# Optimization experiments

Hardware: AMD Instinct MI355X
Metric: run time of the kernel (lower is better)

## Reference

```python
import jax, jax.numpy as jnp
import numpy as np

H = 12          # num_attention_heads
DH = 64         # attention_head_size (768/12)
LDH = 16        # layout head size (DH / channel_shrink_ratio=4)


def _split_heads(x, h, d):
    # [B,S,h*d] -> [B,h,S,d]
    B, S, _ = x.shape
    return x.reshape(B, S, h, d).transpose(0, 2, 1, 3)


def setup_inputs() -> dict:
    key = jax.random.key(0)
    ks = jax.random.split(key, 16)
    B, S, D, LD = 4, 2048, 768, 192
    std = 0.02
    inp = {
        "hidden_states": jax.random.normal(ks[0], (B, S, D), jnp.float32),
        "layout_hidden_states": jax.random.normal(ks[1], (B, S, LD), jnp.float32),
        "attention_mask": jnp.zeros((B, 1, 1, S), jnp.float32),
        # text-stream QKV (weights stored [in, out] so y = x @ W + b)
        "Wq": jax.random.normal(ks[2], (D, D), jnp.float32) * std,
        "bq": jnp.zeros((D,), jnp.float32),
        "Wk": jax.random.normal(ks[3], (D, D), jnp.float32) * std,
        "bk": jnp.zeros((D,), jnp.float32),
        "Wv": jax.random.normal(ks[4], (D, D), jnp.float32) * std,
        "bv": jnp.zeros((D,), jnp.float32),
        # layout-stream QKV
        "LWq": jax.random.normal(ks[5], (LD, LD), jnp.float32) * std,
        "Lbq": jnp.zeros((LD,), jnp.float32),
        "LWk": jax.random.normal(ks[6], (LD, LD), jnp.float32) * std,
        "Lbk": jnp.zeros((LD,), jnp.float32),
        "LWv": jax.random.normal(ks[7], (LD, LD), jnp.float32) * std,
        "Lbv": jnp.zeros((LD,), jnp.float32),
    }
    return inp


def reference(hidden_states, layout_hidden_states, attention_mask,
              Wq, bq, Wk, bk, Wv, bv, LWq, Lbq, LWk, Lbk, LWv, Lbv):
    B, S, D = hidden_states.shape
    LD = layout_hidden_states.shape[-1]

    q = _split_heads(hidden_states @ Wq + bq, H, DH)   # [B,H,S,DH]
    k = _split_heads(hidden_states @ Wk + bk, H, DH)
    v = _split_heads(hidden_states @ Wv + bv, H, DH)
    lq = _split_heads(layout_hidden_states @ LWq + Lbq, H, LDH)  # [B,H,S,LDH]
    lk = _split_heads(layout_hidden_states @ LWk + Lbk, H, LDH)
    lv = _split_heads(layout_hidden_states @ LWv + Lbv, H, LDH)

    # scaled per-stream scores
    scores_t = jnp.einsum('bhqd,bhkd->bhqk', q, k) / np.sqrt(DH).astype(np.float32)
    scores_l = jnp.einsum('bhqd,bhkd->bhqk', lq, lk) / np.sqrt(LDH).astype(np.float32)

    # bidirectional cross-addition (BiACM); layout branch detaches the text scores
    scores_text = scores_t + scores_l + attention_mask
    scores_layout = jax.lax.stop_gradient(scores_t) + scores_l + attention_mask

    probs_t = jax.nn.softmax(scores_text, axis=-1)
    probs_l = jax.nn.softmax(scores_layout, axis=-1)

    ctx = jnp.einsum('bhqk,bhkd->bhqd', probs_t, v)
    ctx = ctx.transpose(0, 2, 1, 3).reshape(B, S, H * DH)       # [B,S,768]
    lctx = jnp.einsum('bhqk,bhkd->bhqd', probs_l, lv)
    lctx = lctx.transpose(0, 2, 1, 3).reshape(B, S, H * LDH)    # [B,S,192]
    return (ctx, lctx)
```

## Files before the change

### kernel.cpp

```cpp
#include <hip/hip_runtime.h>
#include <hip/hip_bf16.h>
#include <cstdint>
#include <math.h>

typedef __attribute__((ext_vector_type(8))) short bf16x8;
typedef __attribute__((ext_vector_type(4))) float f32x4;

#define MFMA16(a, b, c) __builtin_amdgcn_mfma_f32_16x16x32_bf16((a), (b), (c), 0, 0, 0)

static __device__ __forceinline__ unsigned short f2b(float x) {
  __hip_bfloat16 h = __float2bfloat16(x);
  return __builtin_bit_cast(unsigned short, h);
}

#define INVLN2 1.4426950408889634f

__global__ __launch_bounds__(256) void cvt_f32_bf16(const float* __restrict__ s,
                                                    __hip_bfloat16* __restrict__ d, int n) {
  int stride = gridDim.x * 256 * 4;
  for (int i = (blockIdx.x * 256 + threadIdx.x) * 4; i < n; i += stride) {
    float4 v = *(const float4*)(s + i);
    ushort4 o;
    o.x = f2b(v.x); o.y = f2b(v.y); o.z = f2b(v.z); o.w = f2b(v.w);
    *(ushort4*)&d[i] = o;
  }
}

__global__ __launch_bounds__(256) void transpose_cvt(const float* __restrict__ s0,
                                                     const float* __restrict__ s1,
                                                     const float* __restrict__ s2,
                                                     __hip_bfloat16* __restrict__ dst,
                                                     int K, int N, int Npad) {
  __shared__ float tile[32][33];
  int p = blockIdx.z;
  const float* src = (p == 0) ? s0 : (p == 1) ? s1 : s2;
  int n0 = blockIdx.x * 32, k0 = blockIdx.y * 32;
  int tx = threadIdx.x & 31, ty = threadIdx.x >> 5;
  for (int i = ty; i < 32; i += 8) {
    int k = k0 + i, n = n0 + tx;
    tile[i][tx] = (k < K && n < N) ? src[(size_t)k * N + n] : 0.f;
  }
  __syncthreads();
  for (int i = ty; i < 32; i += 8) {
    int n = n0 + i, k = k0 + tx;
    if (n < Npad && k < K)
      dst[(size_t)p * Npad * K + (size_t)n * K + k] = __float2bfloat16(tile[tx][i]);
  }
}

template <int K, int N, int NPAD, int HD, int COFF>
__global__ __launch_bounds__(256, 2) void proj_gemm(
    const __hip_bfloat16* __restrict__ X, const __hip_bfloat16* __restrict__ Wt,
    const float* __restrict__ bq, const float* __restrict__ bk, const float* __restrict__ bv,
    __hip_bfloat16* __restrict__ qc, __hip_bfloat16* __restrict__ kc,
    __hip_bfloat16* __restrict__ vt, float qscale) {
  __shared__ __hip_bfloat16 lA[128 * 32];
  __shared__ __hip_bfloat16 lB[128 * 32];
  const int tid = threadIdx.x, w = tid >> 6, l = tid & 63;
  const int lr = l & 15, lg = l >> 4;
  const int p = blockIdx.z;
  const int m0 = blockIdx.x * 128, n0 = blockIdx.y * 128;
  const __hip_bfloat16* Wp = Wt + (size_t)p * NPAD * K;
  const float* bias = (p == 0) ? bq : (p == 1) ? bk : bv;
  const float scale = (p == 0) ? qscale : 1.0f;

  f32x4 acc[4][4] = {};

  const int srow = (w * 2) * 16 + (l >> 2);
  const int scol = (l & 3) * 8;
  const __hip_bfloat16* gA = X + (size_t)(m0 + srow) * K + scol;
  const __hip_bfloat16* gB = Wp + (size_t)(n0 + srow) * K + scol;
  __hip_bfloat16* dA = lA + (w * 2) * 512;
  __hip_bfloat16* dB = lB + (w * 2) * 512;
  const int wr = w >> 1, wc = w & 1;

  for (int kk = 0; kk < K; kk += 32) {
    __builtin_amdgcn_global_load_lds((const __attribute__((address_space(1))) void*)(gA + kk),
                                     (__attribute__((address_space(3))) void*)dA, 16, 0, 0);
    __builtin_amdgcn_global_load_lds((const __attribute__((address_space(1))) void*)(gA + (size_t)16 * K + kk),
                                     (__attribute__((address_space(3))) void*)(dA + 512), 16, 0, 0);
    __builtin_amdgcn_global_load_lds((const __attribute__((address_space(1))) void*)(gB + kk),
                                     (__attribute__((address_space(3))) void*)dB, 16, 0, 0);
    __builtin_amdgcn_global_load_lds((const __attribute__((address_space(1))) void*)(gB + (size_t)16 * K + kk),
                                     (__attribute__((address_space(3))) void*)(dB + 512), 16, 0, 0);
    __syncthreads();
    bf16x8 af[4], bfr[4];
#pragma unroll
    for (int i = 0; i < 4; i++) af[i] = *(const bf16x8*)(lA + (wr * 64 + i * 16 + lr) * 32 + lg * 8);
#pragma unroll
    for (int j = 0; j < 4; j++) bfr[j] = *(const bf16x8*)(lB + (wc * 64 + j * 16 + lr) * 32 + lg * 8);
#pragma unroll
    for (int i = 0; i < 4; i++)
#pragma unroll
      for (int j = 0; j < 4; j++) acc[i][j] = MFMA16(bfr[j], af[i], acc[i][j]);
    __syncthreads();
  }

#pragma unroll
  for (int j = 0; j < 4; j++) {
    int nb = n0 + wc * 64 + j * 16 + lg * 4;
    if (NPAD > N && nb >= N) continue;
    float4 bv4 = *(const float4*)(bias + nb);
    int hh = nb / HD, d0 = nb % HD;
#pragma unroll
    for (int i = 0; i < 4; i++) {
      int m = m0 + wr * 64 + i * 16 + lr;
      int bb = m >> 11, s = m & 2047;
      if (p == 2) {
        size_t based = ((size_t)(bb * 12 + hh) * 80 + COFF + d0) * 2048 + s;
        vt[based]          = __float2bfloat16(acc[i][j][0] + bv4.x);
        vt[based + 2048]   = __float2bfloat16(acc[i][j][1] + bv4.y);
        vt[based + 4096]   = __float2bfloat16(acc[i][j][2] + bv4.z);
        vt[based + 6144]   = __float2bfloat16(acc[i][j][3] + bv4.w);
      } else {
        size_t base = ((size_t)(bb * 12 + hh) * 2048 + s) * 80 + COFF + d0;
        ushort4 st;
        st.x = f2b((acc[i][j][0] + bv4.x) * scale);
        st.y = f2b((acc[i][j][1] + bv4.y) * scale);
        st.z = f2b((acc[i][j][2] + bv4.z) * scale);
        st.w = f2b((acc[i][j][3] + bv4.w) * scale);
        *(ushort4*)((p == 0 ? qc : kc) + base) = st;
      }
    }
  }
}

__global__ __launch_bounds__(256, 3) void attn_kernel(
    const __hip_bfloat16* __restrict__ qc, const __hip_bfloat16* __restrict__ kc,
    const __hip_bfloat16* __restrict__ vt, const float* __restrict__ mask,
    float* __restrict__ out, float* __restrict__ out2) {
  constexpr int KP = 88;
  constexpr int VP = 72;
  constexpr int SP = 72;
  __shared__ __hip_bfloat16 lK[64 * KP];
  __shared__ __hip_bfloat16 lV[96 * VP];
  __shared__ __hip_bfloat16 lP[4 * 32 * SP];
  const int tid = threadIdx.x, w = tid >> 6, l = tid & 63;
  const int lr = l & 15, lg = l >> 4;
  const int bh = blockIdx.y, b_ = bh / 12, h = bh - b_ * 12;
  const int q0 = blockIdx.x * 128;

  const __hip_bfloat16* gsrc[5];
  int gstep[5];
  __hip_bfloat16* ldst[5];
#pragma unroll
  for (int s = 0; s < 5; ++s) {
    int idx = tid + s * 256;
    if (idx < 640) {
      int r = idx / 10, c = idx - r * 10;
      gsrc[s] = kc + ((size_t)bh * 2048 + r) * 80 + c * 8;
      gstep[s] = 64 * 80;
      ldst[s] = lK + r * KP + c * 8;
    } else {
      int vi = idx - 640;
      int r = vi >> 3, c = vi & 7;
      gsrc[s] = vt + ((size_t)bh * 80 + r) * 2048 + c * 8;
      gstep[s] = 64;
      ldst[s] = lV + r * VP + c * 8;
    }
  }

  const bf16x8 zz = {0, 0, 0, 0, 0, 0, 0, 0};
  bf16x8 aq[2][3];
#pragma unroll
  for (int g = 0; g < 2; ++g) {
    const __hip_bfloat16* qrow = qc + ((size_t)bh * 2048 + q0 + w * 32 + g * 16 + lr) * 80;
    aq[g][0] = *(const bf16x8*)(qrow + lg * 8);
    aq[g][1] = *(const bf16x8*)(qrow + 32 + lg * 8);
    bf16x8 t = *(const bf16x8*)(qrow + 64 + (lg & 1) * 8);
    aq[g][2] = (lg < 2) ? t : zz;
  }

  if (tid < 128) {
    int r = 80 + (tid >> 3), c = tid & 7;
    short v = (r == 80) ? (short)0x3F80 : (short)0;
    bf16x8 x = {v, v, v, v, v, v, v, v};
    *(bf16x8*)(lV + r * VP + c * 8) = x;
  }
  {
    bf16x8 r0[5];
#pragma unroll
    for (int s = 0; s < 5; ++s) r0[s] = *(const bf16x8*)(gsrc[s]);
#pragma unroll
    for (int s = 0; s < 5; ++s) *(bf16x8*)(ldst[s]) = r0[s];
  }
  __syncthreads();

  float mrun[2] = {-INFINITY, -INFINITY};
  f32x4 o[2][6] = {};
  const float* maskb = mask + b_ * 2048;
  __hip_bfloat16* SPw = lP + w * 32 * SP;

  for (int kt = 0; kt < 32; ++kt) {
    int ktn = (kt + 1 < 32) ? kt + 1 : 31;
    bf16x8 pre[5];
#pragma unroll
    for (int s = 0; s < 5; ++s)
      pre[s] = *(const bf16x8*)(gsrc[s] + (size_t)ktn * gstep[s]);

    const int kv0 = kt * 64;

    f32x4 sf[2][4] = {};
#pragma unroll
    for (int f = 0; f < 4; ++f) {
      const __hip_bfloat16* kr = lK + (f * 16 + lr) * KP;
      bf16x8 b0 = *(const bf16x8*)(kr + lg * 8);
      bf16x8 b1 = *(const bf16x8*)(kr + 32 + lg * 8);
      bf16x8 bt = *(const bf16x8*)(kr + 64 + (lg & 1) * 8);
      bf16x8 b2 = (lg < 2) ? bt : zz;
#pragma unroll
      for (int g = 0; g < 2; ++g) {
        sf[g][f] = MFMA16(b0, aq[g][0], sf[g][f]);
        sf[g][f] = MFMA16(b1, aq[g][1], sf[g][f]);
        sf[g][f] = MFMA16(b2, aq[g][2], sf[g][f]);
      }
    }
#pragma unroll
    for (int f = 0; f < 4; ++f) {
      float4 mv = *(const float4*)(maskb + kv0 + f * 16 + lg * 4);
#pragma unroll
      for (int g = 0; g < 2; ++g) {
        sf[g][f][0] += mv.x * INVLN2;
        sf[g][f][1] += mv.y * INVLN2;
        sf[g][f][2] += mv.z * INVLN2;
        sf[g][f][3] += mv.w * INVLN2;
      }
    }
    float tm[2];
#pragma unroll
    for (int g = 0; g < 2; ++g) {
      float a01 = fmaxf(fmaxf(sf[g][0][0], sf[g][0][1]), fmaxf(sf[g][0][2], sf[g][0][3]));
      float a23 = fmaxf(fmaxf(sf[g][1][0], sf[g][1][1]), fmaxf(sf[g][1][2], sf[g][1][3]));
      float a45 = fmaxf(fmaxf(sf[g][2][0], sf[g][2][1]), fmaxf(sf[g][2][2], sf[g][2][3]));
      float a67 = fmaxf(fmaxf(sf[g][3][0], sf[g][3][1]), fmaxf(sf[g][3][2], sf[g][3][3]));
      float m = fmaxf(fmaxf(a01, a23), fmaxf(a45, a67));
      m = fmaxf(m, __shfl_xor(m, 16));
      m = fmaxf(m, __shfl_xor(m, 32));
      tm[g] = m;
    }
    if (__any((tm[0] > mrun[0] + 8.f) || (tm[1] > mrun[1] + 8.f))) {
      float nm0 = fmaxf(mrun[0], tm[0]), nm1 = fmaxf(mrun[1], tm[1]);
      float a0 = exp2f(mrun[0] - nm0), a1 = exp2f(mrun[1] - nm1);
      mrun[0] = nm0; mrun[1] = nm1;
      float aO0[4], aO1[4];
#pragma unroll
      for (int j = 0; j < 4; ++j) {
        aO0[j] = __shfl(a0, lg * 4 + j);
        aO1[j] = __shfl(a1, lg * 4 + j);
      }
#pragma unroll
      for (int c = 0; c < 6; ++c)
#pragma unroll
        for (int j = 0; j < 4; ++j) {
          o[0][c][j] *= aO0[j];
          o[1][c][j] *= aO1[j];
        }
    }
#pragma unroll
    for (int g = 0; g < 2; ++g)
#pragma unroll
      for (int f = 0; f < 4; ++f) {
        ushort4 pk;
        pk.x = f2b(exp2f(sf[g][f][0] - mrun[g]));
        pk.y = f2b(exp2f(sf[g][f][1] - mrun[g]));
        pk.z = f2b(exp2f(sf[g][f][2] - mrun[g]));
        pk.w = f2b(exp2f(sf[g][f][3] - mrun[g]));
        *(ushort4*)(SPw + (g * 16 + lr) * SP + f * 16 + lg * 4) = pk;
      }

#pragma unroll
    for (int t2 = 0; t2 < 2; ++t2) {
      bf16x8 pa0 = *(const bf16x8*)(SPw + lr * SP + t2 * 32 + lg * 8);
      bf16x8 pa1 = *(const bf16x8*)(SPw + (16 + lr) * SP + t2 * 32 + lg * 8);
#pragma unroll
      for (int c = 0; c < 6; ++c) {
        bf16x8 bv_ = *(const bf16x8*)(lV + (c * 16 + lr) * VP + t2 * 32 + lg * 8);
        o[0][c] = MFMA16(pa0, bv_, o[0][c]);
        o[1][c] = MFMA16(pa1, bv_, o[1][c]);
      }
    }
    __syncthreads();
#pragma unroll
    for (int s = 0; s < 5; ++s) *(bf16x8*)(ldst[s]) = pre[s];
    __syncthreads();
  }

#pragma unroll
  for (int g = 0; g < 2; ++g) {
#pragma unroll
    for (int j = 0; j < 4; ++j) {
      float den = __shfl(o[g][5][j], (l & 48));
      float inv = 1.0f / den;
      int qg = q0 + w * 32 + g * 16 + lg * 4 + j;
      float* ob = out + ((size_t)b_ * 2048 + qg) * 768 + h * 64;
#pragma unroll
      for (int c = 0; c < 4; ++c) ob[c * 16 + lr] = o[g][c][j] * inv;
      out2[((size_t)b_ * 2048 + qg) * 192 + h * 16 + lr] = o[g][4][j] * inv;
    }
  }
}

extern "C" void kernel_launch(void* const* d_in, const int* in_sizes, int n_in,
                              void* d_out, int out_size, void* d_ws, size_t ws_size,
                              hipStream_t stream) {
  const float* hidden = (const float*)d_in[0];
  const float* lhidden = (const float*)d_in[1];
  const float* mask = (const float*)d_in[2];
  const float* Wq = (const float*)d_in[3];
  const float* bq = (const float*)d_in[4];
  const float* Wk = (const float*)d_in[5];
  const float* bk = (const float*)d_in[6];
  const float* Wv = (const float*)d_in[7];
  const float* bv = (const float*)d_in[8];
  const float* LWq = (const float*)d_in[9];
  const float* Lbq = (const float*)d_in[10];
  const float* LWk = (const float*)d_in[11];
  const float* Lbk = (const float*)d_in[12];
  const float* LWv = (const float*)d_in[13];
  const float* Lbv = (const float*)d_in[14];

  char* ws = (char*)d_ws;
  __hip_bfloat16* Xb  = (__hip_bfloat16*)(ws + 0);
  __hip_bfloat16* LXb = (__hip_bfloat16*)(ws + 12582912);
  __hip_bfloat16* Wt  = (__hip_bfloat16*)(ws + 15728640);
  __hip_bfloat16* LWt = (__hip_bfloat16*)(ws + 19267584);
  __hip_bfloat16* qcb = (__hip_bfloat16*)(ws + 19562496);
  __hip_bfloat16* kcb = (__hip_bfloat16*)(ws + 35291136);
  __hip_bfloat16* vtb = (__hip_bfloat16*)(ws + 51019776);

  float* out = (float*)d_out;
  float* out2 = out + (size_t)4 * 2048 * 768;

  cvt_f32_bf16<<<2048, 256, 0, stream>>>(hidden, Xb, 6291456);
  cvt_f32_bf16<<<1024, 256, 0, stream>>>(lhidden, LXb, 1572864);
  transpose_cvt<<<dim3(24, 24, 3), 256, 0, stream>>>(Wq, Wk, Wv, Wt, 768, 768, 768);
  transpose_cvt<<<dim3(8, 6, 3), 256, 0, stream>>>(LWq, LWk, LWv, LWt, 192, 192, 256);

  proj_gemm<768, 768, 768, 64, 0><<<dim3(64, 6, 3), 256, 0, stream>>>(
      Xb, Wt, bq, bk, bv, qcb, kcb, vtb, 0.125f * INVLN2);
  proj_gemm<192, 192, 256, 16, 64><<<dim3(64, 2, 3), 256, 0, stream>>>(
      LXb, LWt, Lbq, Lbk, Lbv, qcb, kcb, vtb, 0.25f * INVLN2);

  attn_kernel<<<dim3(16, 48), 256, 0, stream>>>(qcb, kcb, vtb, mask, out, out2);
}
```

Baseline: 319.7 us.

## Rewrite attention loop with 32x32 MFMA, double-buffered LDS and register-resident P

Rewrites the attention kernel to use 32x32x16 bf16 MFMAs instead of 16x16x32, so each wave handles 32 queries with one running max per lane. K tiles are double-buffered in LDS via direct global-to-LDS loads, and V tiles are prefetched into a second buffer. This removes one barrier per iteration and the LDS round-trip for the probability matrix, since the score accumulator layout feeds the PV MFMA directly from registers. LDS use and register pressure change, which may affect occupancy at 3 blocks per CU, and the V staging writes use narrower 8-byte stores.

```diff
diff --git a/kernel.cpp b/kernel.cpp
--- a/kernel.cpp
+++ b/kernel.cpp
@@ -4,13 +4,21 @@
 #include <math.h>
 
 typedef __attribute__((ext_vector_type(8))) short bf16x8;
+typedef __attribute__((ext_vector_type(4))) short bf16x4;
 typedef __attribute__((ext_vector_type(4))) float f32x4;
+typedef __attribute__((ext_vector_type(16))) float f32x16;
 
 #define MFMA16(a, b, c) __builtin_amdgcn_mfma_f32_16x16x32_bf16((a), (b), (c), 0, 0, 0)
+#define MFMA32(a, b, c) __builtin_amdgcn_mfma_f32_32x32x16_bf16((a), (b), (c), 0, 0, 0)
 
 static __device__ __forceinline__ unsigned short f2b(float x) {
   __hip_bfloat16 h = __float2bfloat16(x);
   return __builtin_bit_cast(unsigned short, h);
+}
+
+static __device__ __forceinline__ void gload16(const void* g, void* l) {
+  __builtin_amdgcn_global_load_lds((const __attribute__((address_space(1))) void*)g,
+                                   (__attribute__((address_space(3))) void*)l, 16, 0, 0);
 }
 
 #define INVLN2 1.4426950408889634f
@@ -75,14 +83,10 @@
   const int wr = w >> 1, wc = w & 1;
 
   for (int kk = 0; kk < K; kk += 32) {
-    __builtin_amdgcn_global_load_lds((const __attribute__((address_space(1))) void*)(gA + kk),
-                                     (__attribute__((address_space(3))) void*)dA, 16, 0, 0);
-    __builtin_amdgcn_global_load_lds((const __attribute__((address_space(1))) void*)(gA + (size_t)16 * K + kk),
-                                     (__attribute__((address_space(3))) void*)(dA + 512), 16, 0, 0);
-    __builtin_amdgcn_global_load_lds((const __attribute__((address_space(1))) void*)(gB + kk),
-                                     (__attribute__((address_space(3))) void*)dB, 16, 0, 0);
-    __builtin_amdgcn_global_load_lds((const __attribute__((address_space(1))) void*)(gB + (size_t)16 * K + kk),
-                                     (__attribute__((address_space(3))) void*)(dB + 512), 16, 0, 0);
+    gload16(gA + kk, dA);
+    gload16(gA + (size_t)16 * K + kk, dA + 512);
+    gload16(gB + kk, dB);
+    gload16(gB + (size_t)16 * K + kk, dB + 512);
     __syncthreads();
     bf16x8 af[4], bfr[4];
 #pragma unroll
@@ -129,174 +133,157 @@
     const __hip_bfloat16* __restrict__ qc, const __hip_bfloat16* __restrict__ kc,
     const __hip_bfloat16* __restrict__ vt, const float* __restrict__ mask,
     float* __restrict__ out, float* __restrict__ out2) {
-  constexpr int KP = 88;
-  constexpr int VP = 72;
-  constexpr int SP = 72;
-  __shared__ __hip_bfloat16 lK[64 * KP];
-  __shared__ __hip_bfloat16 lV[96 * VP];
-  __shared__ __hip_bfloat16 lP[4 * 32 * SP];
+  __shared__ __hip_bfloat16 lK[2][10 * 512];
+  __shared__ __hip_bfloat16 lV[2][8 * 776];
   const int tid = threadIdx.x, w = tid >> 6, l = tid & 63;
-  const int lr = l & 15, lg = l >> 4;
+  const int hi = l >> 5, ln = l & 31;
   const int bh = blockIdx.y, b_ = bh / 12, h = bh - b_ * 12;
   const int q0 = blockIdx.x * 128;
 
-  const __hip_bfloat16* gsrc[5];
-  int gstep[5];
-  __hip_bfloat16* ldst[5];
-#pragma unroll
-  for (int s = 0; s < 5; ++s) {
-    int idx = tid + s * 256;
-    if (idx < 640) {
-      int r = idx / 10, c = idx - r * 10;
-      gsrc[s] = kc + ((size_t)bh * 2048 + r) * 80 + c * 8;
-      gstep[s] = 64 * 80;
-      ldst[s] = lK + r * KP + c * 8;
-    } else {
-      int vi = idx - 640;
-      int r = vi >> 3, c = vi & 7;
-      gsrc[s] = vt + ((size_t)bh * 80 + r) * 2048 + c * 8;
-      gstep[s] = 64;
-      ldst[s] = lV + r * VP + c * 8;
-    }
-  }
-
-  const bf16x8 zz = {0, 0, 0, 0, 0, 0, 0, 0};
-  bf16x8 aq[2][3];
-#pragma unroll
-  for (int g = 0; g < 2; ++g) {
-    const __hip_bfloat16* qrow = qc + ((size_t)bh * 2048 + q0 + w * 32 + g * 16 + lr) * 80;
-    aq[g][0] = *(const bf16x8*)(qrow + lg * 8);
-    aq[g][1] = *(const bf16x8*)(qrow + 32 + lg * 8);
-    bf16x8 t = *(const bf16x8*)(qrow + 64 + (lg & 1) * 8);
-    aq[g][2] = (lg < 2) ? t : zz;
-  }
-
-  if (tid < 128) {
-    int r = 80 + (tid >> 3), c = tid & 7;
-    short v = (r == 80) ? (short)0x3F80 : (short)0;
+  const __hip_bfloat16* kbase = kc + ((size_t)bh * 2048 + l) * 80;
+  const __hip_bfloat16* vbase = vt + (size_t)bh * 80 * 2048;
+  const float* maskb = mask + b_ * 2048;
+
+  const int vd0 = tid >> 3, va0 = tid & 7;
+  const int vd1 = (tid + 256) >> 3, va1 = tid & 7;
+  const int vd2 = (tid + 512) >> 3, va2 = tid & 7;
+
+  bf16x8 aq[5];
+  {
+    const __hip_bfloat16* qp = qc + ((size_t)bh * 2048 + q0 + w * 32 + ln) * 80 + hi * 8;
+#pragma unroll
+    for (int t = 0; t < 5; ++t) aq[t] = *(const bf16x8*)(qp + t * 16);
+  }
+
+  {
+    int buf = tid >> 7, g = (tid >> 4) & 7, row = 80 + (tid & 15);
+    short v = (row == 80) ? (short)0x3F80 : (short)0;
     bf16x8 x = {v, v, v, v, v, v, v, v};
-    *(bf16x8*)(lV + r * VP + c * 8) = x;
+    *(bf16x8*)(&lV[buf][g * 776 + row * 8]) = x;
   }
   {
-    bf16x8 r0[5];
-#pragma unroll
-    for (int s = 0; s < 5; ++s) r0[s] = *(const bf16x8*)(gsrc[s]);
-#pragma unroll
-    for (int s = 0; s < 5; ++s) *(bf16x8*)(ldst[s]) = r0[s];
+    const __hip_bfloat16* kg = kbase;
+    gload16(kg + w * 8, &lK[0][w * 512]);
+    gload16(kg + (4 + w) * 8, &lK[0][(4 + w) * 512]);
+    if (w < 2) gload16(kg + (8 + w) * 8, &lK[0][(8 + w) * 512]);
+    bf16x8 v0 = *(const bf16x8*)(vbase + (size_t)vd0 * 2048 + va0 * 8);
+    bf16x8 v1 = *(const bf16x8*)(vbase + (size_t)vd1 * 2048 + va1 * 8);
+    *(bf16x4*)(&lV[0][(va0 & 6) * 776 + vd0 * 8 + (va0 & 1) * 4]) = bf16x4{v0[0], v0[1], v0[2], v0[3]};
+    *(bf16x4*)(&lV[0][((va0 & 6) | 1) * 776 + vd0 * 8 + (va0 & 1) * 4]) = bf16x4{v0[4], v0[5], v0[6], v0[7]};
+    *(bf16x4*)(&lV[0][(va1 & 6) * 776 + vd1 * 8 + (va1 & 1) * 4]) = bf16x4{v1[0], v1[1], v1[2], v1[3]};
+    *(bf16x4*)(&lV[0][((va1 & 6) | 1) * 776 + vd1 * 8 + (va1 & 1) * 4]) = bf16x4{v1[4], v1[5], v1[6], v1[7]};
+    if (tid < 128) {
+      bf16x8 v2 = *(const bf16x8*)(vbase + (size_t)vd2 * 2048 + va2 * 8);
+      *(bf16x4*)(&lV[0][(va2 & 6) * 776 + vd2 * 8 + (va2 & 1) * 4]) = bf16x4{v2[0], v2[1], v2[2], v2[3]};
+      *(bf16x4*)(&lV[0][((va2 & 6) | 1) * 776 + vd2 * 8 + (va2 & 1) * 4]) = bf16x4{v2[4], v2[5], v2[6], v2[7]};
+    }
   }
   __syncthreads();
 
-  float mrun[2] = {-INFINITY, -INFINITY};
-  f32x4 o[2][6] = {};
-  const float* maskb = mask + b_ * 2048;
-  __hip_bfloat16* SPw = lP + w * 32 * SP;
+  float mrun = -INFINITY;
+  f32x16 o0 = {}, o1 = {}, o2 = {};
 
   for (int kt = 0; kt < 32; ++kt) {
-    int ktn = (kt + 1 < 32) ? kt + 1 : 31;
-    bf16x8 pre[5];
-#pragma unroll
-    for (int s = 0; s < 5; ++s)
-      pre[s] = *(const bf16x8*)(gsrc[s] + (size_t)ktn * gstep[s]);
-
+    const int cur = kt & 1, nxt = cur ^ 1;
+    const int kvn = (kt + 1 < 32) ? (kt + 1) * 64 : kt * 64;
     const int kv0 = kt * 64;
 
-    f32x4 sf[2][4] = {};
-#pragma unroll
-    for (int f = 0; f < 4; ++f) {
-      const __hip_bfloat16* kr = lK + (f * 16 + lr) * KP;
-      bf16x8 b0 = *(const bf16x8*)(kr + lg * 8);
-      bf16x8 b1 = *(const bf16x8*)(kr + 32 + lg * 8);
-      bf16x8 bt = *(const bf16x8*)(kr + 64 + (lg & 1) * 8);
-      bf16x8 b2 = (lg < 2) ? bt : zz;
-#pragma unroll
-      for (int g = 0; g < 2; ++g) {
-        sf[g][f] = MFMA16(b0, aq[g][0], sf[g][f]);
-        sf[g][f] = MFMA16(b1, aq[g][1], sf[g][f]);
-        sf[g][f] = MFMA16(b2, aq[g][2], sf[g][f]);
-      }
-    }
-#pragma unroll
-    for (int f = 0; f < 4; ++f) {
-      float4 mv = *(const float4*)(maskb + kv0 + f * 16 + lg * 4);
-#pragma unroll
-      for (int g = 0; g < 2; ++g) {
-        sf[g][f][0] += mv.x * INVLN2;
-        sf[g][f][1] += mv.y * INVLN2;
-        sf[g][f][2] += mv.z * INVLN2;
-        sf[g][f][3] += mv.w * INVLN2;
-      }
-    }
-    float tm[2];
-#pragma unroll
-    for (int g = 0; g < 2; ++g) {
-      float a01 = fmaxf(fmaxf(sf[g][0][0], sf[g][0][1]), fmaxf(sf[g][0][2], sf[g][0][3]));
-      float a23 = fmaxf(fmaxf(sf[g][1][0], sf[g][1][1]), fmaxf(sf[g][1][2], sf[g][1][3]));
-      float a45 = fmaxf(fmaxf(sf[g][2][0], sf[g][2][1]), fmaxf(sf[g][2][2], sf[g][2][3]));
-      float a67 = fmaxf(fmaxf(sf[g][3][0], sf[g][3][1]), fmaxf(sf[g][3][2], sf[g][3][3]));
-      float m = fmaxf(fmaxf(a01, a23), fmaxf(a45, a67));
-      m = fmaxf(m, __shfl_xor(m, 16));
-      m = fmaxf(m, __shfl_xor(m, 32));
-      tm[g] = m;
-    }
-    if (__any((tm[0] > mrun[0] + 8.f) || (tm[1] > mrun[1] + 8.f))) {
-      float nm0 = fmaxf(mrun[0], tm[0]), nm1 = fmaxf(mrun[1], tm[1]);
-      float a0 = exp2f(mrun[0] - nm0), a1 = exp2f(mrun[1] - nm1);
-      mrun[0] = nm0; mrun[1] = nm1;
-      float aO0[4], aO1[4];
-#pragma unroll
-      for (int j = 0; j < 4; ++j) {
-        aO0[j] = __shfl(a0, lg * 4 + j);
-        aO1[j] = __shfl(a1, lg * 4 + j);
-      }
-#pragma unroll
-      for (int c = 0; c < 6; ++c)
-#pragma unroll
-        for (int j = 0; j < 4; ++j) {
-          o[0][c][j] *= aO0[j];
-          o[1][c][j] *= aO1[j];
-        }
-    }
-#pragma unroll
-    for (int g = 0; g < 2; ++g)
-#pragma unroll
-      for (int f = 0; f < 4; ++f) {
-        ushort4 pk;
-        pk.x = f2b(exp2f(sf[g][f][0] - mrun[g]));
-        pk.y = f2b(exp2f(sf[g][f][1] - mrun[g]));
-        pk.z = f2b(exp2f(sf[g][f][2] - mrun[g]));
-        pk.w = f2b(exp2f(sf[g][f][3] - mrun[g]));
-        *(ushort4*)(SPw + (g * 16 + lr) * SP + f * 16 + lg * 4) = pk;
-      }
-
-#pragma unroll
-    for (int t2 = 0; t2 < 2; ++t2) {
-      bf16x8 pa0 = *(const bf16x8*)(SPw + lr * SP + t2 * 32 + lg * 8);
-      bf16x8 pa1 = *(const bf16x8*)(SPw + (16 + lr) * SP + t2 * 32 + lg * 8);
-#pragma unroll
-      for (int c = 0; c < 6; ++c) {
-        bf16x8 bv_ = *(const bf16x8*)(lV + (c * 16 + lr) * VP + t2 * 32 + lg * 8);
-        o[0][c] = MFMA16(pa0, bv_, o[0][c]);
-        o[1][c] = MFMA16(pa1, bv_, o[1][c]);
-      }
+    {
+      const __hip_bfloat16* kg = kbase + (size_t)kvn * 80;
+      gload16(kg + w * 8, &lK[nxt][w * 512]);
+      gload16(kg + (4 + w) * 8, &lK[nxt][(4 + w) * 512]);
+      if (w < 2) gload16(kg + (8 + w) * 8, &lK[nxt][(8 + w) * 512]);
+    }
+    bf16x8 v0 = *(const bf16x8*)(vbase + (size_t)vd0 * 2048 + kvn + va0 * 8);
+    bf16x8 v1 = *(const bf16x8*)(vbase + (size_t)vd1 * 2048 + kvn + va1 * 8);
+    bf16x8 v2;
+    if (tid < 128) v2 = *(const bf16x8*)(vbase + (size_t)vd2 * 2048 + kvn + va2 * 8);
+
+    const __hip_bfloat16* lKc = &lK[cur][0];
+    f32x16 sf0 = {}, sf1 = {};
+#pragma unroll
+    for (int t = 0; t < 5; ++t) {
+      bf16x8 ak0 = *(const bf16x8*)(lKc + (t * 2 + hi) * 512 + ln * 8);
+      bf16x8 ak1 = *(const bf16x8*)(lKc + (t * 2 + hi) * 512 + (32 + ln) * 8);
+      sf0 = MFMA32(ak0, aq[t], sf0);
+      sf1 = MFMA32(ak1, aq[t], sf1);
+    }
+
+    float s_[2][16];
+#pragma unroll
+    for (int q = 0; q < 4; ++q) {
+      float4 m0 = *(const float4*)(maskb + kv0 + 4 * hi + q * 8);
+      float4 m1 = *(const float4*)(maskb + kv0 + 32 + 4 * hi + q * 8);
+#pragma unroll
+      for (int c = 0; c < 4; ++c) {
+        s_[0][q * 4 + c] = sf0[q * 4 + c] + ((const float*)&m0)[c] * INVLN2;
+        s_[1][q * 4 + c] = sf1[q * 4 + c] + ((const float*)&m1)[c] * INVLN2;
+      }
+    }
+
+    float tm = s_[0][0];
+#pragma unroll
+    for (int r = 1; r < 16; ++r) tm = fmaxf(tm, s_[0][r]);
+#pragma unroll
+    for (int r = 0; r < 16; ++r) tm = fmaxf(tm, s_[1][r]);
+    tm = fmaxf(tm, __shfl_xor(tm, 32));
+    if (__any(tm > mrun + 8.f)) {
+      float nm = fmaxf(mrun, tm);
+      float alpha = exp2f(mrun - nm);
+      mrun = nm;
+#pragma unroll
+      for (int r = 0; r < 16; ++r) {
+        float a = __shfl(alpha, (r & 3) + 8 * (r >> 2) + 4 * hi);
+        o0[r] *= a; o1[r] *= a; o2[r] *= a;
+      }
+    }
+
+    bf16x8 pa[2][2];
+#pragma unroll
+    for (int kb = 0; kb < 2; ++kb)
+#pragma unroll
+      for (int ks = 0; ks < 2; ++ks) {
+        bf16x8 pk;
+#pragma unroll
+        for (int j = 0; j < 8; ++j)
+          pk[j] = (short)f2b(exp2f(s_[kb][ks * 8 + j] - mrun));
+        pa[kb][ks] = pk;
+      }
+
+    const __hip_bfloat16* lVc = &lV[cur][0];
+#pragma unroll
+    for (int kb = 0; kb < 2; ++kb)
+#pragma unroll
+      for (int ks = 0; ks < 2; ++ks) {
+        const int g = (kb * 2 + ks) * 2 + hi;
+        bf16x8 bv0 = *(const bf16x8*)(lVc + g * 776 + ln * 8);
+        bf16x8 bv1 = *(const bf16x8*)(lVc + g * 776 + (32 + ln) * 8);
+        bf16x8 bv2 = *(const bf16x8*)(lVc + g * 776 + (64 + ln) * 8);
+        o0 = MFMA32(pa[kb][ks], bv0, o0);
+        o1 = MFMA32(pa[kb][ks], bv1, o1);
+        o2 = MFMA32(pa[kb][ks], bv2, o2);
+      }
+
+    *(bf16x4*)(&lV[nxt][(va0 & 6) * 776 + vd0 * 8 + (va0 & 1) * 4]) = bf16x4{v0[0], v0[1], v0[2], v0[3]};
+    *(bf16x4*)(&lV[nxt][((va0 & 6) | 1) * 776 + vd0 * 8 + (va0 & 1) * 4]) = bf16x4{v0[4], v0[5], v0[6], v0[7]};
+    *(bf16x4*)(&lV[nxt][(va1 & 6) * 776 + vd1 * 8 + (va1 & 1) * 4]) = bf16x4{v1[0], v1[1], v1[2], v1[3]};
+    *(bf16x4*)(&lV[nxt][((va1 & 6) | 1) * 776 + vd1 * 8 + (va1 & 1) * 4]) = bf16x4{v1[4], v1[5], v1[6], v1[7]};
+    if (tid < 128) {
+      *(bf16x4*)(&lV[nxt][(va2 & 6) * 776 + vd2 * 8 + (va2 & 1) * 4]) = bf16x4{v2[0], v2[1], v2[2], v2[3]};
+      *(bf16x4*)(&lV[nxt][((va2 & 6) | 1) * 776 + vd2 * 8 + (va2 & 1) * 4]) = bf16x4{v2[4], v2[5], v2[6], v2[7]};
     }
     __syncthreads();
-#pragma unroll
-    for (int s = 0; s < 5; ++s) *(bf16x8*)(ldst[s]) = pre[s];
-    __syncthreads();
-  }
-
-#pragma unroll
-  for (int g = 0; g < 2; ++g) {
-#pragma unroll
-    for (int j = 0; j < 4; ++j) {
-      float den = __shfl(o[g][5][j], (l & 48));
-      float inv = 1.0f / den;
-      int qg = q0 + w * 32 + g * 16 + lg * 4 + j;
-      float* ob = out + ((size_t)b_ * 2048 + qg) * 768 + h * 64;
-#pragma unroll
-      for (int c = 0; c < 4; ++c) ob[c * 16 + lr] = o[g][c][j] * inv;
-      out2[((size_t)b_ * 2048 + qg) * 192 + h * 16 + lr] = o[g][4][j] * inv;
-    }
+  }
+
+#pragma unroll
+  for (int r = 0; r < 16; ++r) {
+    float den = __shfl(o2[r], 16 | (l & 32));
+    float inv = 1.0f / den;
+    int qg = q0 + w * 32 + (r & 3) + 8 * (r >> 2) + 4 * hi;
+    size_t rowb = (size_t)b_ * 2048 + qg;
+    out[rowb * 768 + h * 64 + ln] = o0[r] * inv;
+    out[rowb * 768 + h * 64 + 32 + ln] = o1[r] * inv;
+    if (ln < 16) out2[rowb * 192 + h * 16 + ln] = o2[r] * inv;
   }
 }
 
```

Measured after the change: 291.6 us. 8.8% less time.
